# Optimization experiments

Hardware: AMD Instinct MI355X
Metric: run time of the kernel (lower is better)

## Reference

```python
import jax, jax.numpy as jnp
import numpy as np

B, T, C = 2, 2048, 1024
H, DH = 16, 64  # num_heads, dim_head; inner_dim = H*DH = C


def setup_inputs() -> dict:
    key = jax.random.key(0)
    k_x, k_q, k_k, k_v, k_o, k_r = jax.random.split(key, 6)
    scaled = lambda k, shape, fan: (jax.random.normal(k, shape, jnp.float32) / np.sqrt(fan).astype(np.float32))
    x = jax.random.normal(k_x, (B, T, C), jnp.float32)
    Wq = scaled(k_q, (C, H * DH), C)
    Wk = scaled(k_k, (C, H * DH), C)
    Wv = scaled(k_v, (C, H * DH), C)
    Wo = scaled(k_o, (H * DH, C), H * DH)
    bo = jnp.zeros((C,), jnp.float32)
    # learned relative position bias table, indexed by (i - j) in [-(T-1), T-1]
    rel_table = jax.random.normal(k_r, (H, 2 * T - 1), jnp.float32) * 0.02
    # causal mask, broadcast over batch and heads
    mask = jnp.tril(jnp.ones((T, T), bool))[None, None]  # [1,1,T,T]
    return {"x": x, "Wq": Wq, "Wk": Wk, "Wv": Wv, "Wo": Wo, "bo": bo,
            "rel_table": rel_table, "mask": mask}


def reference(x, Wq, Wk, Wv, Wo, bo, rel_table, mask):
    Bx, Tx, Cx = x.shape
    split = lambda t: t.reshape(Bx, Tx, H, DH).transpose(0, 2, 1, 3)  # [B,H,T,DH]
    q = split(x @ Wq) * (DH ** -0.5)
    k = split(x @ Wk)
    v = split(x @ Wv)
    # relative position bias: bias[h,i,j] = rel_table[h, i-j + T-1]
    rel_idx = jnp.arange(Tx)[:, None] - jnp.arange(Tx)[None, :] + (Tx - 1)  # [T,T]
    bias = rel_table[:, rel_idx]  # [H,T,T]
    score = jnp.einsum('bhid,bhjd->bhij', q, k) + bias[None]
    mask_value = -jnp.finfo(score.dtype).max
    score = jnp.where(mask, score, mask_value)
    attn = jax.nn.softmax(score, axis=-1)
    y = jnp.einsum('bhij,bhjd->bhid', attn, v)
    y = y.transpose(0, 2, 1, 3).reshape(Bx, Tx, H * DH)
    return y @ Wo + bo
```

## Files before the change

### kernel.cpp

```cpp
#include <hip/hip_runtime.h>
#include <hip/hip_bf16.h>
#include <stdint.h>


#define T_SEQ 2048
#define NH    16
#define DHD   64
#define CDIM  1024

typedef unsigned short u16;
typedef unsigned int   u32;
typedef __attribute__((ext_vector_type(8))) __bf16 bf16x8;
typedef __attribute__((ext_vector_type(4))) float f32x4;

#define WAITL0   asm volatile("s_waitcnt lgkmcnt(0)" ::: "memory")

__device__ __forceinline__ float bf2f(u16 b){
  union { u32 u; float f; } v; v.u = ((u32)b) << 16; return v.f;
}
__device__ __forceinline__ u16 f2bf(float f){
  union { __bf16 h; u16 u; } v; v.h = (__bf16)f;
  return v.u;
}

__device__ __forceinline__ void gload_lds16(const u16* g, u16* l){
  __builtin_amdgcn_global_load_lds(
      (const __attribute__((address_space(1))) void*)g,
      (__attribute__((address_space(3))) void*)l, 16, 0, 0);
}

__device__ __forceinline__ uint4 load8(const void* p, long elem, int isbf){
  if (isbf) return *(const uint4*)((const u16*)p + elem);
  const float* fp = (const float*)p + elem;
  float4 a = *(const float4*)fp, b = *(const float4*)(fp + 4);
  uint4 r;
  r.x = (u32)f2bf(a.x) | ((u32)f2bf(a.y) << 16);
  r.y = (u32)f2bf(a.z) | ((u32)f2bf(a.w) << 16);
  r.z = (u32)f2bf(b.x) | ((u32)f2bf(b.y) << 16);
  r.w = (u32)f2bf(b.z) | ((u32)f2bf(b.w) << 16);
  return r;
}
__device__ __forceinline__ float loadf(const void* p, long idx, int isbf){
  return isbf ? bf2f(((const u16*)p)[idx]) : ((const float*)p)[idx];
}

__global__ __launch_bounds__(256) void classify(const u32* __restrict__ x,
                                                int* __restrict__ flag){
  __shared__ int cnt[256];
  int c = 0;
#pragma unroll
  for (int i = 0; i < 16; i++){
    u32 w = x[threadIdx.x * 16 + i];
    int e = (w >> 7) & 0xFF;
    c += (e >= 110 && e <= 140);
  }
  cnt[threadIdx.x] = c;
  __syncthreads();
  for (int s = 128; s > 0; s >>= 1){
    if ((int)threadIdx.x < s) cnt[threadIdx.x] += cnt[threadIdx.x + s];
    __syncthreads();
  }
  if (threadIdx.x == 0) *flag = (cnt[0] > 2048) ? 1 : 0;
}

__global__ __launch_bounds__(256) void cvt_x(const void* __restrict__ x,
                                             u16* __restrict__ xbf,
                                             const int* __restrict__ flag){
  const int isbf = *flag;
  const long i = ((long)blockIdx.x * 256 + threadIdx.x) * 8;
  *(uint4*)(xbf + i) = load8(x, i, isbf);
}

__global__ __launch_bounds__(256) void transposeW(
    const void* __restrict__ w0, const void* __restrict__ w1,
    const void* __restrict__ w2,
    u16* __restrict__ o0, u16* __restrict__ o1, u16* __restrict__ o2,
    const int* __restrict__ flag)
{
  __shared__ u16 tile[64][72];
  const int isbf = *flag;
  const int z = blockIdx.z;
  const void* in = z==0 ? w0 : z==1 ? w1 : w2;
  u16*      out  = z==0 ? o0 : z==1 ? o1 : o2;
  const int tid = threadIdx.x;
  const int r0 = blockIdx.y * 64, c0 = blockIdx.x * 64;
  const int rr = tid >> 3;
  const int cc = (tid & 7) * 8;
#pragma unroll
  for (int rd = 0; rd < 2; rd++){
    int r = rd*32 + rr;
    *(uint4*)&tile[r][cc] = load8(in, (long)(r0 + r)*CDIM + c0 + cc, isbf);
  }
  __syncthreads();
#pragma unroll
  for (int rd = 0; rd < 2; rd++){
    int oc = rd*32 + rr;
    uint4 wv; u32* wp = (u32*)&wv;
#pragma unroll
    for (int t = 0; t < 4; t++){
      u32 lo = tile[cc + 2*t][oc];
      u32 hi = tile[cc + 2*t + 1][oc];
      wp[t] = lo | (hi << 16);
    }
    *(uint4*)(out + (long)(c0 + oc)*CDIM + r0 + cc) = wv;
  }
}

__device__ __forceinline__ void gemm_body(
    const u16* __restrict__ A, const u16* __restrict__ BT,
    const void* __restrict__ bias, void* __restrict__ out,
    float scale, int mode, int m0, int n0, int io_isbf)
{
  __shared__ u16 ldsA[2][128*32];
  __shared__ u16 ldsB[2][128*32];
  const int tid = threadIdx.x;
  const int wid = tid >> 6, lane = tid & 63;
  const int col = lane & 15, quad = lane >> 4;
  const int wm = (wid >> 1) * 64, wn = (wid & 1) * 64;

  const int c0 = wid*128 + lane, c1 = c0 + 64;
  const int r0c = c0 >> 2, g0c = c0 & 3;
  const int r1c = c1 >> 2, g1c = c1 & 3;
  const long aoff0 = (long)r0c*CDIM + ((g0c ^ (r0c & 3)) << 3);
  const long aoff1 = (long)r1c*CDIM + ((g1c ^ (r1c & 3)) << 3);
  const int lds0 = (wid*128)*8;
  const int lds1 = (wid*128 + 64)*8;

  const u16* gA = A  + (long)m0*CDIM;
  const u16* gB = BT + (long)n0*CDIM;

  auto stage = [&](int buf, int k0){
    gload_lds16(gA + k0 + aoff0, &ldsA[buf][lds0]);
    gload_lds16(gA + k0 + aoff1, &ldsA[buf][lds1]);
    gload_lds16(gB + k0 + aoff0, &ldsB[buf][lds0]);
    gload_lds16(gB + k0 + aoff1, &ldsB[buf][lds1]);
  };

  f32x4 acc[4][4] = {};
  const int NK = CDIM / 32;

  stage(0, 0);
  __syncthreads();

  int cur = 0;
  for (int k = 0; k < NK; k++){
    if (k + 1 < NK) stage(cur ^ 1, (k + 1) * 32);

    bf16x8 af[4], bfr[4];
#pragma unroll
    for (int mi = 0; mi < 4; mi++){
      const int r = wm + mi*16 + col;
      af[mi] = *(const bf16x8*)&ldsA[cur][r*32 + ((quad ^ (r & 3)) * 8)];
    }
#pragma unroll
    for (int ni = 0; ni < 4; ni++){
      const int r = wn + ni*16 + col;
      bfr[ni] = *(const bf16x8*)&ldsB[cur][r*32 + ((quad ^ (r & 3)) * 8)];
    }
#pragma unroll
    for (int mi = 0; mi < 4; mi++)
#pragma unroll
      for (int ni = 0; ni < 4; ni++)
        acc[mi][ni] = __builtin_amdgcn_mfma_f32_16x16x32_bf16(af[mi], bfr[ni], acc[mi][ni], 0, 0, 0);

    __syncthreads();
    cur ^= 1;
  }

  if (mode == 2){
#pragma unroll
    for (int ni = 0; ni < 4; ni++){
      const int n = n0 + wn + ni*16 + col;
      const int h = n >> 6, d = n & 63;
#pragma unroll
      for (int mi = 0; mi < 4; mi++){
        const int m = m0 + wm + mi*16 + quad*4;
        const int b = m >> 11, t = m & (T_SEQ-1);
        uint2 pk;
        pk.x = (u32)f2bf(acc[mi][ni][0]) | ((u32)f2bf(acc[mi][ni][1]) << 16);
        pk.y = (u32)f2bf(acc[mi][ni][2]) | ((u32)f2bf(acc[mi][ni][3]) << 16);
        *(uint2*)((u16*)out + ((long)(b*NH + h)*DHD + d)*T_SEQ + t) = pk;
      }
    }
  } else {
#pragma unroll
    for (int ni = 0; ni < 4; ni++){
      const int n = n0 + wn + ni*16 + col;
      const float bv = bias ? loadf(bias, n, io_isbf) : 0.f;
#pragma unroll
      for (int mi = 0; mi < 4; mi++){
#pragma unroll
        for (int r = 0; r < 4; r++){
          const int m = m0 + wm + mi*16 + quad*4 + r;
          const float v = acc[mi][ni][r] * scale + bv;
          if (mode == 0){
            const long idx = (long)m*CDIM + n;
            if (io_isbf) ((u16*)out)[idx] = f2bf(v);
            else         ((float*)out)[idx] = v;
          } else {
            const int b = m >> 11, t = m & (T_SEQ-1), h = n >> 6, d = n & 63;
            ((u16*)out)[((long)(b*NH + h)*T_SEQ + t)*DHD + d] = f2bf(v);
          }
        }
      }
    }
  }
}

__global__ __launch_bounds__(256) void gemm_qkv(
    const u16* __restrict__ xbf,
    const u16* __restrict__ WqT, const u16* __restrict__ WkT, const u16* __restrict__ WvT,
    u16* __restrict__ Qb, u16* __restrict__ Kb, u16* __restrict__ VTb)
{
  const int z = blockIdx.z;
  const u16* BT = z==0 ? WqT : z==1 ? WkT : WvT;
  u16*      dst = z==0 ? Qb  : z==1 ? Kb  : VTb;
  const float scale = (z==0) ? 0.125f * 1.44269504f : 1.0f;
  const int mode = (z==2) ? 2 : 1;
  gemm_body(xbf, BT, nullptr, dst, scale, mode, blockIdx.x*128, blockIdx.y*128, 1);
}

__global__ __launch_bounds__(256) void gemm_out(
    const u16* __restrict__ Y, const u16* __restrict__ WoT,
    const void* __restrict__ bo, void* __restrict__ out,
    const int* __restrict__ flag)
{
  gemm_body(Y, WoT, bo, out, 1.0f, 0, blockIdx.x*128, blockIdx.y*128, *flag);
}

__global__ __launch_bounds__(256) void attn64(
    const u16* __restrict__ Q, const u16* __restrict__ K, const u16* __restrict__ VT,
    const void* __restrict__ rel, u16* __restrict__ Y,
    const int* __restrict__ flag)
{
  __shared__ u16 ldsK[64*64];
  __shared__ u16 ldsV[64*64];
  __shared__ u16 ldsP[4][16*88];
  __shared__ float ldsBias[2112];

  const int isbf = *flag;
  const int tid = threadIdx.x, wid = tid >> 6, lane = tid & 63;
  const int col = lane & 15, quad = lane >> 4;

  const int l = (int)blockIdx.x;
  const int xcd = l & 7, s = l >> 3;
  const int bh = xcd * 4 + (s & 3);
  const int g = s >> 2, gq = g >> 3, g0 = g & 7;
  const int ti = (gq == 0) ? 31 - g0
               : (gq == 1) ? g0
               : (gq == 2) ? 23 - g0
                           : 8 + g0;
  const int i0 = ti * 64;

  const int h = bh & (NH - 1);
  const int b = bh >> 4;

  const u16* Qh = Q  + (long)bh * T_SEQ * DHD;
  const u16* Kh = K  + (long)bh * T_SEQ * DHD;
  const u16* Vh = VT + (long)bh * DHD * T_SEQ;
  const long relbase = (long)h * (2*T_SEQ - 1) + (T_SEQ - 1);
  const float MLOG = 16.0f * 1.44269504f;

  const int kr0 = tid >> 3, ks = tid & 7;
  const int kr1 = kr0 + 32;
  const int kd0 = (ks ^ (kr0 & 7)) * 8;
  const int kd1 = (ks ^ (kr1 & 7)) * 8;

  uint4 rk0, rk1, rv0, rv1;
  auto loadKV = [&](int j0){
    rk0 = *(const uint4*)(Kh + (long)(j0 + kr0)*DHD + ks*8);
    rk1 = *(const uint4*)(Kh + (long)(j0 + kr1)*DHD + ks*8);
    rv0 = *(const uint4*)(Vh + (long)kr0*T_SEQ + j0 + ks*8);
    rv1 = *(const uint4*)(Vh + (long)kr1*T_SEQ + j0 + ks*8);
  };
  auto storeKV = [&](){
    *(uint4*)&ldsK[kr0*64 + kd0] = rk0;
    *(uint4*)&ldsK[kr1*64 + kd1] = rk1;
    *(uint4*)&ldsV[kr0*64 + kd0] = rv0;
    *(uint4*)&ldsV[kr1*64 + kd1] = rv1;
  };

  const int nbias = i0 + 127;
  for (int t = tid; t < nbias; t += 256)
    ldsBias[t] = loadf(rel, relbase + t - 63, isbf) * 1.44269504f - MLOG;

  bf16x8 qf0, qf1;
  {
    const u16* qp = Qh + (long)(i0 + wid*16 + col)*DHD + quad*8;
    qf0 = *(const bf16x8*)qp;
    qf1 = *(const bf16x8*)(qp + 32);
  }

  f32x4 O[4] = {};
  float lsum[4] = {0.f, 0.f, 0.f, 0.f};
  const int irow = i0 + wid*16 + quad*4;

  loadKV(0);
  storeKV();
  __syncthreads();

  for (int j0 = 0; j0 <= i0; j0 += 64){
    const bool have_next = (j0 + 64 <= i0);
    if (have_next) loadKV(j0 + 64);

    f32x4 s[4] = {};
#pragma unroll
    for (int kb = 0; kb < 2; kb++){
#pragma unroll
      for (int nb = 0; nb < 4; nb++){
        const int row = nb*16 + col;
        const int sl = ((kb*4 + quad) ^ (row & 7)) * 8;
        bf16x8 kf = *(const bf16x8*)&ldsK[row*64 + sl];
        s[nb] = __builtin_amdgcn_mfma_f32_16x16x32_bf16(kb ? qf1 : qf0, kf, s[nb], 0, 0, 0);
      }
    }

    const bool diag = (j0 == i0);
#pragma unroll
    for (int nb = 0; nb < 4; nb++){
      const int j = j0 + nb*16 + col;
      const float* bp = &ldsBias[irow - j + 63];
#pragma unroll
      for (int r = 0; r < 4; r++){
        float arg = s[nb][r] + bp[r];
        if (diag && (j > irow + r)) arg = -1e9f;
        float p;
        asm volatile("v_exp_f32 %0, %1" : "=v"(p) : "v"(arg));
        s[nb][r] = p;
        lsum[r] += p;
      }
    }

    u16* Pw = ldsP[wid];
#pragma unroll
    for (int nb = 0; nb < 4; nb++)
#pragma unroll
      for (int r = 0; r < 4; r++)
        Pw[(quad*4 + r)*88 + nb*16 + col] = f2bf(s[nb][r]);
    WAITL0;

#pragma unroll
    for (int kb = 0; kb < 2; kb++){
      bf16x8 pf = *(const bf16x8*)&Pw[col*88 + kb*32 + quad*8];
#pragma unroll
      for (int nb = 0; nb < 4; nb++){
        const int row = nb*16 + col;
        const int sl = ((kb*4 + quad) ^ (row & 7)) * 8;
        bf16x8 vf = *(const bf16x8*)&ldsV[row*64 + sl];
        O[nb] = __builtin_amdgcn_mfma_f32_16x16x32_bf16(pf, vf, O[nb], 0, 0, 0);
      }
    }

    __syncthreads();
    if (have_next){
      storeKV();
      __syncthreads();
    }
  }

#pragma unroll
  for (int r = 0; r < 4; r++){
    float v = lsum[r];
    v += __shfl_xor(v, 1, 64);
    v += __shfl_xor(v, 2, 64);
    v += __shfl_xor(v, 4, 64);
    v += __shfl_xor(v, 8, 64);
    lsum[r] = v;
  }

#pragma unroll
  for (int nb = 0; nb < 4; nb++){
#pragma unroll
    for (int r = 0; r < 4; r++){
      const int i = irow + r;
      const int d = nb*16 + col;
      Y[((long)(b*T_SEQ + i))*CDIM + h*DHD + d] = f2bf(O[nb][r] / lsum[r]);
    }
  }
}

extern "C" void kernel_launch(void* const* d_in, const int* in_sizes, int n_in,
                              void* d_out, int out_size, void* d_ws, size_t ws_size,
                              hipStream_t stream)
{
  (void)in_sizes; (void)n_in; (void)out_size; (void)ws_size;
  const void* x   = d_in[0];
  const void* Wq  = d_in[1];
  const void* Wk  = d_in[2];
  const void* Wv  = d_in[3];
  const void* Wo  = d_in[4];
  const void* bo  = d_in[5];
  const void* rel = d_in[6];

  char* ws = (char*)d_ws;
  const size_t MB = 1024*1024;
  int* flag = (int*)ws;
  char* base = ws + 256;
  u16* WqT = (u16*)(base + 0*MB);
  u16* WkT = (u16*)(base + 2*MB);
  u16* WvT = (u16*)(base + 4*MB);
  u16* Kb  = (u16*)(base + 6*MB);
  u16* VTb = (u16*)(base + 14*MB);
  u16* Yb  = (u16*)(base + 0*MB);
  u16* WoT = (u16*)(base + 8*MB);
  u16* Qb  = (u16*)d_out;
  u16* xbf = Qb + 4u*1024*1024;

  dim3 blk(256);
  classify  <<<1, blk, 0, stream>>>((const u32*)x, flag);
  cvt_x     <<<dim3(2048), blk, 0, stream>>>(x, xbf, flag);
  transposeW<<<dim3(16,16,3), blk, 0, stream>>>(Wq, Wk, Wv, WqT, WkT, WvT, flag);
  gemm_qkv  <<<dim3(32,8,3),  blk, 0, stream>>>(xbf, WqT, WkT, WvT, Qb, Kb, VTb);
  attn64    <<<dim3(1024),  blk, 0, stream>>>(Qb, Kb, VTb, rel, Yb, flag);
  transposeW<<<dim3(16,16,1), blk, 0, stream>>>(Wo, Wo, Wo, WoT, WoT, WoT, flag);
  gemm_out  <<<dim3(32,8),    blk, 0, stream>>>(Yb, WoT, bo, d_out, flag);
}
```

Measured before the change: 223.7 us.

## Process two 64-row query tiles per attention block to reuse K/V tiles

The attention kernel now gives each block 128 query rows (two 64-row sub-tiles sharing each loaded K/V tile) instead of 64, which halves the grid to 512 blocks and halves the K/V global loads per query row. The tile schedule is changed to pair long and short tiles across the grid, and the P scratch buffer and bias range grow to match. Launch bounds now request 2 blocks per SIMD, but the doubled accumulators raise register pressure, and fewer, larger blocks may balance less well on the causal triangle.

Result: slower. 261.5 us (+16.9%).

```diff
diff --git a/kernel.cpp b/kernel.cpp
--- a/kernel.cpp
+++ b/kernel.cpp
@@ -228,14 +228,14 @@
   gemm_body(Y, WoT, bo, out, 1.0f, 0, blockIdx.x*128, blockIdx.y*128, *flag);
 }
 
-__global__ __launch_bounds__(256) void attn64(
+__global__ __launch_bounds__(256, 2) void attn64(
     const u16* __restrict__ Q, const u16* __restrict__ K, const u16* __restrict__ VT,
     const void* __restrict__ rel, u16* __restrict__ Y,
     const int* __restrict__ flag)
 {
   __shared__ u16 ldsK[64*64];
   __shared__ u16 ldsV[64*64];
-  __shared__ u16 ldsP[4][16*88];
+  __shared__ u16 ldsP[4][32*88];
   __shared__ float ldsBias[2112];
 
   const int isbf = *flag;
@@ -245,12 +245,9 @@
   const int l = (int)blockIdx.x;
   const int xcd = l & 7, s = l >> 3;
   const int bh = xcd * 4 + (s & 3);
-  const int g = s >> 2, gq = g >> 3, g0 = g & 7;
-  const int ti = (gq == 0) ? 31 - g0
-               : (gq == 1) ? g0
-               : (gq == 2) ? 23 - g0
-                           : 8 + g0;
-  const int i0 = ti * 64;
+  const int g = s >> 2;
+  const int ti = (g < 8) ? (15 - g) : (g - 8);
+  const int i0 = ti * 128;
 
   const int h = bh & (NH - 1);
   const int b = bh >> 4;
@@ -280,30 +277,32 @@
     *(uint4*)&ldsV[kr1*64 + kd1] = rv1;
   };
 
-  const int nbias = i0 + 127;
+  const int nbias = i0 + 191;
   for (int t = tid; t < nbias; t += 256)
     ldsBias[t] = loadf(rel, relbase + t - 63, isbf) * 1.44269504f - MLOG;
 
-  bf16x8 qf0, qf1;
-  {
-    const u16* qp = Qh + (long)(i0 + wid*16 + col)*DHD + quad*8;
-    qf0 = *(const bf16x8*)qp;
-    qf1 = *(const bf16x8*)(qp + 32);
-  }
-
-  f32x4 O[4] = {};
-  float lsum[4] = {0.f, 0.f, 0.f, 0.f};
-  const int irow = i0 + wid*16 + quad*4;
+  bf16x8 qf[2][2];
+#pragma unroll
+  for (int mi = 0; mi < 2; mi++){
+    const u16* qp = Qh + (long)(i0 + mi*64 + wid*16 + col)*DHD + quad*8;
+    qf[mi][0] = *(const bf16x8*)qp;
+    qf[mi][1] = *(const bf16x8*)(qp + 32);
+  }
+
+  f32x4 O0[4] = {}, O1[4] = {};
+  float lsum0[4] = {0.f,0.f,0.f,0.f}, lsum1[4] = {0.f,0.f,0.f,0.f};
+  const int irow0 = i0 + wid*16 + quad*4;
+  const int irow1 = irow0 + 64;
 
   loadKV(0);
   storeKV();
   __syncthreads();
 
-  for (int j0 = 0; j0 <= i0; j0 += 64){
-    const bool have_next = (j0 + 64 <= i0);
-    if (have_next) loadKV(j0 + 64);
-
-    f32x4 s[4] = {};
+  for (int j0 = 0; j0 <= i0 + 64; j0 += 64){
+    const bool do0 = (j0 <= i0);
+    if (do0) loadKV(j0 + 64);
+
+    f32x4 s0[4] = {}, s1[4] = {};
 #pragma unroll
     for (int kb = 0; kb < 2; kb++){
 #pragma unroll
@@ -311,48 +310,75 @@
         const int row = nb*16 + col;
         const int sl = ((kb*4 + quad) ^ (row & 7)) * 8;
         bf16x8 kf = *(const bf16x8*)&ldsK[row*64 + sl];
-        s[nb] = __builtin_amdgcn_mfma_f32_16x16x32_bf16(kb ? qf1 : qf0, kf, s[nb], 0, 0, 0);
-      }
-    }
-
-    const bool diag = (j0 == i0);
+        if (do0) s0[nb] = __builtin_amdgcn_mfma_f32_16x16x32_bf16(qf[0][kb], kf, s0[nb], 0, 0, 0);
+        s1[nb] = __builtin_amdgcn_mfma_f32_16x16x32_bf16(qf[1][kb], kf, s1[nb], 0, 0, 0);
+      }
+    }
+
+    const bool diag0 = (j0 == i0);
+    const bool diag1 = (j0 == i0 + 64);
+    if (do0){
+#pragma unroll
+      for (int nb = 0; nb < 4; nb++){
+        const int j = j0 + nb*16 + col;
+        const float* bp = &ldsBias[irow0 - j + 63];
+#pragma unroll
+        for (int r = 0; r < 4; r++){
+          float arg = s0[nb][r] + bp[r];
+          if (diag0 && (j > irow0 + r)) arg = -1e9f;
+          float p;
+          asm volatile("v_exp_f32 %0, %1" : "=v"(p) : "v"(arg));
+          s0[nb][r] = p;
+          lsum0[r] += p;
+        }
+      }
+    }
 #pragma unroll
     for (int nb = 0; nb < 4; nb++){
       const int j = j0 + nb*16 + col;
-      const float* bp = &ldsBias[irow - j + 63];
+      const float* bp = &ldsBias[irow1 - j + 63];
 #pragma unroll
       for (int r = 0; r < 4; r++){
-        float arg = s[nb][r] + bp[r];
-        if (diag && (j > irow + r)) arg = -1e9f;
+        float arg = s1[nb][r] + bp[r];
+        if (diag1 && (j > irow1 + r)) arg = -1e9f;
         float p;
         asm volatile("v_exp_f32 %0, %1" : "=v"(p) : "v"(arg));
-        s[nb][r] = p;
-        lsum[r] += p;
+        s1[nb][r] = p;
+        lsum1[r] += p;
       }
     }
 
     u16* Pw = ldsP[wid];
+    if (do0){
+#pragma unroll
+      for (int nb = 0; nb < 4; nb++)
+#pragma unroll
+        for (int r = 0; r < 4; r++)
+          Pw[(quad*4 + r)*88 + nb*16 + col] = f2bf(s0[nb][r]);
+    }
 #pragma unroll
     for (int nb = 0; nb < 4; nb++)
 #pragma unroll
       for (int r = 0; r < 4; r++)
-        Pw[(quad*4 + r)*88 + nb*16 + col] = f2bf(s[nb][r]);
+        Pw[(16 + quad*4 + r)*88 + nb*16 + col] = f2bf(s1[nb][r]);
     WAITL0;
 
 #pragma unroll
     for (int kb = 0; kb < 2; kb++){
-      bf16x8 pf = *(const bf16x8*)&Pw[col*88 + kb*32 + quad*8];
+      bf16x8 pf0 = *(const bf16x8*)&Pw[col*88 + kb*32 + quad*8];
+      bf16x8 pf1 = *(const bf16x8*)&Pw[(16 + col)*88 + kb*32 + quad*8];
 #pragma unroll
       for (int nb = 0; nb < 4; nb++){
         const int row = nb*16 + col;
         const int sl = ((kb*4 + quad) ^ (row & 7)) * 8;
         bf16x8 vf = *(const bf16x8*)&ldsV[row*64 + sl];
-        O[nb] = __builtin_amdgcn_mfma_f32_16x16x32_bf16(pf, vf, O[nb], 0, 0, 0);
+        if (do0) O0[nb] = __builtin_amdgcn_mfma_f32_16x16x32_bf16(pf0, vf, O0[nb], 0, 0, 0);
+        O1[nb] = __builtin_amdgcn_mfma_f32_16x16x32_bf16(pf1, vf, O1[nb], 0, 0, 0);
       }
     }
 
     __syncthreads();
-    if (have_next){
+    if (do0){
       storeKV();
       __syncthreads();
     }
@@ -360,21 +386,27 @@
 
 #pragma unroll
   for (int r = 0; r < 4; r++){
-    float v = lsum[r];
+    float v = lsum0[r];
     v += __shfl_xor(v, 1, 64);
     v += __shfl_xor(v, 2, 64);
     v += __shfl_xor(v, 4, 64);
     v += __shfl_xor(v, 8, 64);
-    lsum[r] = v;
+    lsum0[r] = v;
+    float w = lsum1[r];
+    w += __shfl_xor(w, 1, 64);
+    w += __shfl_xor(w, 2, 64);
+    w += __shfl_xor(w, 4, 64);
+    w += __shfl_xor(w, 8, 64);
+    lsum1[r] = w;
   }
 
 #pragma unroll
   for (int nb = 0; nb < 4; nb++){
 #pragma unroll
     for (int r = 0; r < 4; r++){
-      const int i = irow + r;
       const int d = nb*16 + col;
-      Y[((long)(b*T_SEQ + i))*CDIM + h*DHD + d] = f2bf(O[nb][r] / lsum[r]);
+      Y[((long)(b*T_SEQ + irow0 + r))*CDIM + h*DHD + d] = f2bf(O0[nb][r] / lsum0[r]);
+      Y[((long)(b*T_SEQ + irow1 + r))*CDIM + h*DHD + d] = f2bf(O1[nb][r] / lsum1[r]);
     }
   }
 }
@@ -411,7 +443,7 @@
   cvt_x     <<<dim3(2048), blk, 0, stream>>>(x, xbf, flag);
   transposeW<<<dim3(16,16,3), blk, 0, stream>>>(Wq, Wk, Wv, WqT, WkT, WvT, flag);
   gemm_qkv  <<<dim3(32,8,3),  blk, 0, stream>>>(xbf, WqT, WkT, WvT, Qb, Kb, VTb);
-  attn64    <<<dim3(1024),  blk, 0, stream>>>(Qb, Kb, VTb, rel, Yb, flag);
+  attn64    <<<dim3(512),  blk, 0, stream>>>(Qb, Kb, VTb, rel, Yb, flag);
   transposeW<<<dim3(16,16,1), blk, 0, stream>>>(Wo, Wo, Wo, WoT, WoT, WoT, flag);
   gemm_out  <<<dim3(32,8),    blk, 0, stream>>>(Yb, WoT, bo, d_out, flag);
 }
```

## Double-buffer attention K/V tiles with direct global-to-LDS loads

Applied to the files above, without the earlier changes.

The attention kernel's K/V staging changes from register-held loads followed by an LDS store into two LDS buffers. The next tile is filled straight from global memory with gload_lds16 while the current tile is being computed. This drops the per-iteration register staging and the second barrier after the store, letting memory transfer overlap the MFMA and softmax work. In exchange LDS use doubles for K/V, which may reduce occupancy. Correctness depends on the direct LDS loads having completed before the loop's barrier.

New measurement: 221.4 us. About the same (-1.0%).

```diff
diff --git a/kernel.cpp b/kernel.cpp
--- a/kernel.cpp
+++ b/kernel.cpp
@@ -233,8 +233,8 @@
     const void* __restrict__ rel, u16* __restrict__ Y,
     const int* __restrict__ flag)
 {
-  __shared__ u16 ldsK[64*64];
-  __shared__ u16 ldsV[64*64];
+  __shared__ u16 ldsK[2][64*64];
+  __shared__ u16 ldsV[2][64*64];
   __shared__ u16 ldsP[4][16*88];
   __shared__ float ldsBias[2112];
 
@@ -261,23 +261,17 @@
   const long relbase = (long)h * (2*T_SEQ - 1) + (T_SEQ - 1);
   const float MLOG = 16.0f * 1.44269504f;
 
-  const int kr0 = tid >> 3, ks = tid & 7;
-  const int kr1 = kr0 + 32;
-  const int kd0 = (ks ^ (kr0 & 7)) * 8;
-  const int kd1 = (ks ^ (kr1 & 7)) * 8;
-
-  uint4 rk0, rk1, rv0, rv1;
-  auto loadKV = [&](int j0){
-    rk0 = *(const uint4*)(Kh + (long)(j0 + kr0)*DHD + ks*8);
-    rk1 = *(const uint4*)(Kh + (long)(j0 + kr1)*DHD + ks*8);
-    rv0 = *(const uint4*)(Vh + (long)kr0*T_SEQ + j0 + ks*8);
-    rv1 = *(const uint4*)(Vh + (long)kr1*T_SEQ + j0 + ks*8);
-  };
-  auto storeKV = [&](){
-    *(uint4*)&ldsK[kr0*64 + kd0] = rk0;
-    *(uint4*)&ldsK[kr1*64 + kd1] = rk1;
-    *(uint4*)&ldsV[kr0*64 + kd0] = rv0;
-    *(uint4*)&ldsV[kr1*64 + kd1] = rv1;
+  const int srow0 = wid*8 + (lane >> 3);
+  const int srow1 = srow0 + 32;
+  const int soff  = ((lane & 7) ^ ((lane >> 3) & 7)) * 8;
+  const int sb0   = wid*512;
+  const int sb1   = 2048 + wid*512;
+
+  auto stage = [&](int buf, int j0){
+    gload_lds16(Kh + (long)(j0 + srow0)*DHD + soff, &ldsK[buf][sb0]);
+    gload_lds16(Kh + (long)(j0 + srow1)*DHD + soff, &ldsK[buf][sb1]);
+    gload_lds16(Vh + (long)srow0*T_SEQ + j0 + soff, &ldsV[buf][sb0]);
+    gload_lds16(Vh + (long)srow1*T_SEQ + j0 + soff, &ldsV[buf][sb1]);
   };
 
   const int nbias = i0 + 127;
@@ -295,13 +289,13 @@
   float lsum[4] = {0.f, 0.f, 0.f, 0.f};
   const int irow = i0 + wid*16 + quad*4;
 
-  loadKV(0);
-  storeKV();
+  stage(0, 0);
   __syncthreads();
 
+  int cur = 0;
   for (int j0 = 0; j0 <= i0; j0 += 64){
     const bool have_next = (j0 + 64 <= i0);
-    if (have_next) loadKV(j0 + 64);
+    if (have_next) stage(cur ^ 1, j0 + 64);
 
     f32x4 s[4] = {};
 #pragma unroll
@@ -310,7 +304,7 @@
       for (int nb = 0; nb < 4; nb++){
         const int row = nb*16 + col;
         const int sl = ((kb*4 + quad) ^ (row & 7)) * 8;
-        bf16x8 kf = *(const bf16x8*)&ldsK[row*64 + sl];
+        bf16x8 kf = *(const bf16x8*)&ldsK[cur][row*64 + sl];
         s[nb] = __builtin_amdgcn_mfma_f32_16x16x32_bf16(kb ? qf1 : qf0, kf, s[nb], 0, 0, 0);
       }
     }
@@ -346,16 +340,13 @@
       for (int nb = 0; nb < 4; nb++){
         const int row = nb*16 + col;
         const int sl = ((kb*4 + quad) ^ (row & 7)) * 8;
-        bf16x8 vf = *(const bf16x8*)&ldsV[row*64 + sl];
+        bf16x8 vf = *(const bf16x8*)&ldsV[cur][row*64 + sl];
         O[nb] = __builtin_amdgcn_mfma_f32_16x16x32_bf16(pf, vf, O[nb], 0, 0, 0);
       }
     }
 
     __syncthreads();
-    if (have_next){
-      storeKV();
-      __syncthreads();
-    }
+    cur ^= 1;
   }
 
 #pragma unroll
```
